# Kernel optimization log

Hardware: AMD Instinct MI355X
Metric: run time of the kernel (lower is better)

The kernel has to match this reference:

```python
import jax, jax.numpy as jnp
import numpy as np

N = 8192       # node_num
F_IN = 256     # src_feature
F_OUT = 128    # out_feature
NEG_SLOPE = 0.2  # standard GAT leakyrelu slope
MASK_VAL = -1e12


def setup_inputs() -> dict:
    key = jax.random.key(0)
    k1, k2, k3, k4, k5, k6 = jax.random.split(key, 6)
    x = jax.random.normal(k1, (N, F_IN), dtype=jnp.float32)
    adj = jax.random.randint(k2, (N, N), 0, 2, dtype=jnp.int32)  # 0/1 adjacency mask
    # xavier-uniform-like scales
    W = jax.random.normal(k3, (F_IN, F_OUT), dtype=jnp.float32) * np.float32(1.0 / np.sqrt(F_IN))
    a1 = jax.random.normal(k4, (F_OUT,), dtype=jnp.float32) * np.float32(0.1)  # att[:F_OUT]
    a2 = jax.random.normal(k5, (F_OUT,), dtype=jnp.float32) * np.float32(0.1)  # att[F_OUT:]
    bias = jax.random.normal(k6, (F_OUT,), dtype=jnp.float32) * np.float32(0.1)
    return {"x": x, "adj": adj, "W": W, "a1": a1, "a2": a2, "bias": bias}


def reference(x, adj, W, a1, a2, bias):
    # h = x @ W1  (src_h == dst_h for int src_dst_feature)
    h = x @ W  # [N, F_OUT]
    # e[i,j] = leakyrelu(att^T [h_i || h_j]) decomposed as (h@a1)_i + (h@a2)_j
    s_src = h @ a1  # [N]
    s_dst = h @ a2  # [N]
    e = jax.nn.leaky_relu(s_src[:, None] + s_dst[None, :], NEG_SLOPE)  # [N, N]
    masked = jnp.where(adj > 0, e, jnp.float32(MASK_VAL))
    attention = jax.nn.softmax(masked, axis=1)  # [N, N]
    # dropout in eval mode = identity; aggregate neighbor features
    out = attention @ h + bias  # [N, F_OUT]
    return out
```

## Files before the change

kernel.cpp:

```cpp
#include <hip/hip_runtime.h>
#include <cstdint>
#include <cstddef>

#define NN 8192
#define FIN 256
#define FOUT 128
#define SLOPE 0.2f
#define SHIFT 8.0f

typedef float f32x4 __attribute__((ext_vector_type(4)));
typedef __bf16 bf16x8 __attribute__((ext_vector_type(8)));
typedef int i32x4 __attribute__((ext_vector_type(4)));
typedef unsigned int u32x4 __attribute__((ext_vector_type(4)));
typedef unsigned int u32x2 __attribute__((ext_vector_type(2)));

__device__ __forceinline__ unsigned short f2bf(float f) {
  return __builtin_bit_cast(unsigned short, (__bf16)f);
}
__device__ __forceinline__ float bf2f(unsigned short u) {
  return (float)__builtin_bit_cast(__bf16, u);
}

__device__ __forceinline__ void async_cp16(void* lds, const void* g) {
  __builtin_amdgcn_global_load_lds(
      (const __attribute__((address_space(1))) void*)g,
      (__attribute__((address_space(3))) void*)lds, 16, 0, 0);
}

__global__ __launch_bounds__(256, 4) void k_hw(const float* __restrict__ x,
                                               const float* __restrict__ W,
                                               const float* __restrict__ a1,
                                               const float* __restrict__ a2,
                                               unsigned short* __restrict__ ht,
                                               float* __restrict__ Etab,
                                               unsigned short* __restrict__ FbfF,
                                               unsigned short* __restrict__ FbfF2) {
  __shared__ float xs[8][256];
  __shared__ unsigned short tile[128][8];
  const int tid = threadIdx.x;
  const int rowbase = blockIdx.x * 8;

  #pragma unroll
  for (int it = 0; it < 2; ++it) {
    int fi = it * 1024 + tid * 4;
    int r = fi >> 8, k = fi & 255;
    *(f32x4*)&xs[r][k] = *(const f32x4*)(x + (size_t)(rowbase + r) * FIN + k);
  }
  __syncthreads();

  const int r = tid >> 5;
  const int cg = tid & 31;
  f32x4 acc = {0.f, 0.f, 0.f, 0.f};

  #pragma unroll 8
  for (int k = 0; k < FIN; ++k) {
    f32x4 wv = *(const f32x4*)(W + k * FOUT + cg * 4);
    float xv = xs[r][k];
    acc[0] += xv * wv[0];
    acc[1] += xv * wv[1];
    acc[2] += xv * wv[2];
    acc[3] += xv * wv[3];
  }

  #pragma unroll
  for (int c = 0; c < 4; ++c) tile[cg * 4 + c][r] = f2bf(acc[c]);

  f32x4 av1 = *(const f32x4*)(a1 + cg * 4);
  f32x4 av2 = *(const f32x4*)(a2 + cg * 4);
  float s1 = acc[0] * av1[0] + acc[1] * av1[1] + acc[2] * av1[2] + acc[3] * av1[3];
  float s2 = acc[0] * av2[0] + acc[1] * av2[1] + acc[2] * av2[2] + acc[3] * av2[3];
  #pragma unroll
  for (int off = 16; off > 0; off >>= 1) {
    s1 += __shfl_xor(s1, off, 64);
    s2 += __shfl_xor(s2, off, 64);
  }
  if (cg == 0) {
    const int row = rowbase + r;
    float c0 = s1 + SHIFT;
    float c = fmaxf(c0, SLOPE * c0);
    Etab[(size_t)row * 2]     = __expf(s1 - c);
    Etab[(size_t)row * 2 + 1] = __expf(SLOPE * s1 - c);
    FbfF[row]  = f2bf(__expf(s2));
    FbfF2[row] = f2bf(__expf(SLOPE * s2));
  }
  __syncthreads();

  if (tid < 128) {
    u32x4 v = *(const u32x4*)&tile[tid][0];
    *(u32x4*)(ht + (size_t)tid * NN + rowbase) = v;
  }
}

__global__ __launch_bounds__(256, 2) void k_gat(const int* __restrict__ adj,
                                                const unsigned short* __restrict__ ht,
                                                const float* __restrict__ Etab,
                                                const unsigned short* __restrict__ FbfF,
                                                const unsigned short* __restrict__ FbfF2,
                                                const float* __restrict__ bias,
                                                float* __restrict__ out) {
  __shared__ int sA[2][16 * 64];
  __shared__ unsigned short sH[2][128 * 64];
  __shared__ unsigned short sF[2][128];
  __shared__ unsigned short sAF[2][1024];

  const int tid = threadIdx.x;
  const int wave = tid >> 6;
  const int lane = tid & 63;
  const int quad = lane >> 4;
  const int m = lane & 15;
  const int rowbase = blockIdx.x * 16;

  bf16x8 pm, pinv, pones;
  #pragma unroll
  for (int jj = 0; jj < 8; ++jj) {
    pm[jj] = (__bf16)(float)m;
    pinv[jj] = (__bf16)0.03125f;
    pones[jj] = (__bf16)1.0f;
  }
  f32x4 z = {0.f, 0.f, 0.f, 0.f};
  f32x4 rp = __builtin_amdgcn_mfma_f32_16x16x32_bf16(pm, pinv, z, 0, 0, 0);
  f32x4 cp = __builtin_amdgcn_mfma_f32_16x16x32_bf16(pinv, pm, z, 0, 0, 0);
  int rowmap[4], colmap[4];
  #pragma unroll
  for (int r = 0; r < 4; ++r) {
    rowmap[r] = ((int)(rp[r] + 0.5f)) & 15;
    colmap[r] = ((int)(cp[r] + 0.5f)) & 15;
  }

  const int b_half = tid & 1;
  const int b_lane = (tid >> 1) & 63;
  const int b_k32  = tid >> 7;
  const int b_m    = b_lane & 15;
  const int b_quad = b_lane >> 4;
  const int b_jl   = b_k32 * 32 + b_quad * 8 + b_half * 4;
  const int b_slot = (b_jl >> 2) ^ b_m;
  const float Eb  = Etab[(size_t)(rowbase + b_m) * 2];
  const float E2b = Etab[(size_t)(rowbase + b_m) * 2 + 1];

  const int t0 = wave * 2, t1 = wave * 2 + 1;
  f32x4 acc0 = z, acc1 = z, den = z;

  const unsigned short* srcH[4];
  #pragma unroll
  for (int il = 0; il < 4; ++il) {
    const int i = wave * 4 + il;
    const int f = i * 8 + (lane >> 3);
    const int g = (lane & 7) ^ (lane >> 3);
    srcH[il] = ht + (size_t)f * NN + g * 8;
  }
  const int* srcA[2] = {nullptr, nullptr};
  int slotA[2] = {0, 0};
  if (wave >= 2) {
    #pragma unroll
    for (int q = 0; q < 2; ++q) {
      const int il = (wave - 2) * 2 + q;
      const int r = il * 4 + (lane >> 4);
      const int g = (lane & 15) ^ r;
      slotA[q] = il;
      srcA[q] = adj + (size_t)(rowbase + r) * NN + g * 4;
    }
  }
  const unsigned short* srcF = nullptr;
  if (wave == 1) {
    srcF = (lane < 8) ? (FbfF + lane * 8) : (FbfF2 + (lane - 8) * 8);
  }

  auto stage = [&](int b) {
    #pragma unroll
    for (int il = 0; il < 4; ++il) {
      async_cp16(&sH[b][(wave * 4 + il) * 512], srcH[il]);
      srcH[il] += 64;
    }
    if (wave >= 2) {
      #pragma unroll
      for (int q = 0; q < 2; ++q) {
        async_cp16(&sA[b][slotA[q] * 256], srcA[q]);
        srcA[q] += 64;
      }
    } else if (wave == 1 && lane < 16) {
      async_cp16(&sF[b][0], srcF);
      srcF += 64;
    }
  };

  stage(0);

  for (int c = 0; c < 128; ++c) {
    const int cs = c & 1, ns = cs ^ 1;

    __syncthreads();
    if (c + 1 < 128) stage(ns);

    {
      i32x4 av = *(const i32x4*)&sA[cs][b_m * 64 + b_slot * 4];
      unsigned long long fq = *(const unsigned long long*)&sF[cs][b_jl];
      unsigned long long gq = *(const unsigned long long*)&sF[cs][64 + b_jl];
      unsigned afp0 = 0, afp1 = 0;
      #pragma unroll
      for (int e = 0; e < 4; ++e) {
        const float F = bf2f((unsigned short)(fq >> (16 * e)));
        const float G = bf2f((unsigned short)(gq >> (16 * e)));
        const float w = fmaxf(Eb * F, E2b * G);
        const unsigned wb = av[e] ? (unsigned)f2bf(w) : 0u;
        if (e < 2) afp0 |= wb << (16 * e);
        else       afp1 |= wb << (16 * (e - 2));
      }
      u32x2 pkt; pkt[0] = afp0; pkt[1] = afp1;
      *(u32x2*)&sAF[cs][tid * 4] = pkt;
    }

    __builtin_amdgcn_s_waitcnt(0xC07F);
    __builtin_amdgcn_s_barrier();

    #pragma unroll
    for (int k32 = 0; k32 < 2; ++k32) {
      bf16x8 af = __builtin_bit_cast(bf16x8,
          *(const u32x4*)&sAF[cs][k32 * 512 + lane * 8]);
      const int s0 = (k32 * 4 + quad) ^ (m & 7);
      bf16x8 b0 = __builtin_bit_cast(bf16x8,
          *(const u32x4*)&sH[cs][(t0 * 16 + m) * 64 + s0 * 8]);
      bf16x8 b1 = __builtin_bit_cast(bf16x8,
          *(const u32x4*)&sH[cs][(t1 * 16 + m) * 64 + s0 * 8]);
      acc0 = __builtin_amdgcn_mfma_f32_16x16x32_bf16(af, b0, acc0, 0, 0, 0);
      acc1 = __builtin_amdgcn_mfma_f32_16x16x32_bf16(af, b1, acc1, 0, 0, 0);
      den  = __builtin_amdgcn_mfma_f32_16x16x32_bf16(af, pones, den, 0, 0, 0);
    }
  }

  #pragma unroll
  for (int r = 0; r < 4; ++r) {
    const float inv = 1.0f / den[r];
    const int orow = rowbase + rowmap[r];
    const int c0 = t0 * 16 + colmap[r];
    const int c1 = t1 * 16 + colmap[r];
    out[(size_t)orow * FOUT + c0] = acc0[r] * inv + bias[c0];
    out[(size_t)orow * FOUT + c1] = acc1[r] * inv + bias[c1];
  }
}

extern "C" void kernel_launch(void* const* d_in, const int* in_sizes, int n_in,
                              void* d_out, int out_size, void* d_ws, size_t ws_size,
                              hipStream_t stream) {
  const float* x    = (const float*)d_in[0];
  const int*   adj  = (const int*)d_in[1];
  const float* W    = (const float*)d_in[2];
  const float* a1   = (const float*)d_in[3];
  const float* a2   = (const float*)d_in[4];
  const float* bias = (const float*)d_in[5];
  float* out = (float*)d_out;

  char* ws = (char*)d_ws;
  unsigned short* ht = (unsigned short*)ws;
  float* Etab = (float*)(ws + (size_t)2 * 1024 * 1024);
  unsigned short* FbfF =
      (unsigned short*)(ws + (size_t)2 * 1024 * 1024 + 64 * 1024);
  unsigned short* FbfF2 = FbfF + NN;

  k_hw<<<NN / 8, 256, 0, stream>>>(x, W, a1, a2, ht, Etab, FbfF, FbfF2);
  k_gat<<<NN / 16, 256, 0, stream>>>(adj, ht, Etab, FbfF, FbfF2, bias, out);
}
```

Before: 480.1 us.

## Process 32 rows per block with 512 threads and load h tiles directly into registers

The attention-aggregation kernel now handles 32 output rows per block with 8 waves. Each wave owns 16 output features and loads its bf16 h fragment straight from global memory into registers, prefetched one chunk ahead, instead of staging h through shared memory. This halves how often h is re-read per output row and removes the shared-memory h buffer and its LDS reads. In exchange there are fewer blocks (256 instead of 512, occupancy 1 block of 512 threads), and the direct global loads are uncoalesced row-strided reads whose latency is hidden only by the one-step register prefetch.

```diff
diff --git a/kernel.cpp b/kernel.cpp
--- a/kernel.cpp
+++ b/kernel.cpp
@@ -91,24 +91,23 @@
   }
 }
 
-__global__ __launch_bounds__(256, 2) void k_gat(const int* __restrict__ adj,
+__global__ __launch_bounds__(512, 1) void k_gat(const int* __restrict__ adj,
                                                 const unsigned short* __restrict__ ht,
                                                 const float* __restrict__ Etab,
                                                 const unsigned short* __restrict__ FbfF,
                                                 const unsigned short* __restrict__ FbfF2,
                                                 const float* __restrict__ bias,
                                                 float* __restrict__ out) {
-  __shared__ int sA[2][16 * 64];
-  __shared__ unsigned short sH[2][128 * 64];
+  __shared__ int sA[2][32 * 64];
   __shared__ unsigned short sF[2][128];
-  __shared__ unsigned short sAF[2][1024];
+  __shared__ unsigned short sAF[2][2048];
 
   const int tid = threadIdx.x;
   const int wave = tid >> 6;
   const int lane = tid & 63;
   const int quad = lane >> 4;
   const int m = lane & 15;
-  const int rowbase = blockIdx.x * 16;
+  const int rowbase = blockIdx.x * 32;
 
   bf16x8 pm, pinv, pones;
   #pragma unroll
@@ -129,70 +128,56 @@
 
   const int b_half = tid & 1;
   const int b_lane = (tid >> 1) & 63;
-  const int b_k32  = tid >> 7;
+  const int b_k32  = (tid >> 7) & 1;
+  const int b_rg   = tid >> 8;
   const int b_m    = b_lane & 15;
   const int b_quad = b_lane >> 4;
+  const int b_row  = b_rg * 16 + b_m;
   const int b_jl   = b_k32 * 32 + b_quad * 8 + b_half * 4;
   const int b_slot = (b_jl >> 2) ^ b_m;
-  const float Eb  = Etab[(size_t)(rowbase + b_m) * 2];
-  const float E2b = Etab[(size_t)(rowbase + b_m) * 2 + 1];
-
-  const int t0 = wave * 2, t1 = wave * 2 + 1;
-  f32x4 acc0 = z, acc1 = z, den = z;
-
-  const unsigned short* srcH[4];
-  #pragma unroll
-  for (int il = 0; il < 4; ++il) {
-    const int i = wave * 4 + il;
-    const int f = i * 8 + (lane >> 3);
-    const int g = (lane & 7) ^ (lane >> 3);
-    srcH[il] = ht + (size_t)f * NN + g * 8;
-  }
-  const int* srcA[2] = {nullptr, nullptr};
-  int slotA[2] = {0, 0};
-  if (wave >= 2) {
-    #pragma unroll
-    for (int q = 0; q < 2; ++q) {
-      const int il = (wave - 2) * 2 + q;
-      const int r = il * 4 + (lane >> 4);
-      const int g = (lane & 15) ^ r;
-      slotA[q] = il;
-      srcA[q] = adj + (size_t)(rowbase + r) * NN + g * 4;
-    }
-  }
+  const float Eb  = Etab[(size_t)(rowbase + b_row) * 2];
+  const float E2b = Etab[(size_t)(rowbase + b_row) * 2 + 1];
+
+  f32x4 acc[2] = {z, z}, den[2] = {z, z};
+
+  const int a_r = wave * 4 + (lane >> 4);
+  const int a_g = (lane & 15) ^ (a_r & 15);
+  const int* srcA = adj + (size_t)(rowbase + a_r) * NN + a_g * 4;
   const unsigned short* srcF = nullptr;
-  if (wave == 1) {
+  if (wave == 0) {
     srcF = (lane < 8) ? (FbfF + lane * 8) : (FbfF2 + (lane - 8) * 8);
   }
 
   auto stage = [&](int b) {
-    #pragma unroll
-    for (int il = 0; il < 4; ++il) {
-      async_cp16(&sH[b][(wave * 4 + il) * 512], srcH[il]);
-      srcH[il] += 64;
-    }
-    if (wave >= 2) {
-      #pragma unroll
-      for (int q = 0; q < 2; ++q) {
-        async_cp16(&sA[b][slotA[q] * 256], srcA[q]);
-        srcA[q] += 64;
-      }
-    } else if (wave == 1 && lane < 16) {
+    async_cp16(&sA[b][wave * 256], srcA);
+    srcA += 64;
+    if (wave == 0 && lane < 16) {
       async_cp16(&sF[b][0], srcF);
       srcF += 64;
     }
   };
 
+  const unsigned short* srcB = ht + (size_t)(wave * 16 + m) * NN + quad * 8;
+
   stage(0);
-
+  u32x4 bcur0 = *(const u32x4*)(srcB);
+  u32x4 bcur1 = *(const u32x4*)(srcB + 32);
+
+  #pragma unroll 2
   for (int c = 0; c < 128; ++c) {
     const int cs = c & 1, ns = cs ^ 1;
 
     __syncthreads();
     if (c + 1 < 128) stage(ns);
 
+    u32x4 bnxt0 = bcur0, bnxt1 = bcur1;
+    if (c + 1 < 128) {
+      bnxt0 = *(const u32x4*)(srcB + (c + 1) * 64);
+      bnxt1 = *(const u32x4*)(srcB + (c + 1) * 64 + 32);
+    }
+
     {
-      i32x4 av = *(const i32x4*)&sA[cs][b_m * 64 + b_slot * 4];
+      i32x4 av = *(const i32x4*)&sA[cs][b_row * 64 + b_slot * 4];
       unsigned long long fq = *(const unsigned long long*)&sF[cs][b_jl];
       unsigned long long gq = *(const unsigned long long*)&sF[cs][64 + b_jl];
       unsigned afp0 = 0, afp1 = 0;
@@ -214,27 +199,29 @@
 
     #pragma unroll
     for (int k32 = 0; k32 < 2; ++k32) {
-      bf16x8 af = __builtin_bit_cast(bf16x8,
-          *(const u32x4*)&sAF[cs][k32 * 512 + lane * 8]);
-      const int s0 = (k32 * 4 + quad) ^ (m & 7);
-      bf16x8 b0 = __builtin_bit_cast(bf16x8,
-          *(const u32x4*)&sH[cs][(t0 * 16 + m) * 64 + s0 * 8]);
-      bf16x8 b1 = __builtin_bit_cast(bf16x8,
-          *(const u32x4*)&sH[cs][(t1 * 16 + m) * 64 + s0 * 8]);
-      acc0 = __builtin_amdgcn_mfma_f32_16x16x32_bf16(af, b0, acc0, 0, 0, 0);
-      acc1 = __builtin_amdgcn_mfma_f32_16x16x32_bf16(af, b1, acc1, 0, 0, 0);
-      den  = __builtin_amdgcn_mfma_f32_16x16x32_bf16(af, pones, den, 0, 0, 0);
-    }
-  }
-
-  #pragma unroll
-  for (int r = 0; r < 4; ++r) {
-    const float inv = 1.0f / den[r];
-    const int orow = rowbase + rowmap[r];
-    const int c0 = t0 * 16 + colmap[r];
-    const int c1 = t1 * 16 + colmap[r];
-    out[(size_t)orow * FOUT + c0] = acc0[r] * inv + bias[c0];
-    out[(size_t)orow * FOUT + c1] = acc1[r] * inv + bias[c1];
+      const bf16x8 bf = __builtin_bit_cast(bf16x8, k32 ? bcur1 : bcur0);
+      #pragma unroll
+      for (int rg = 0; rg < 2; ++rg) {
+        bf16x8 af = __builtin_bit_cast(bf16x8,
+            *(const u32x4*)&sAF[cs][rg * 1024 + k32 * 512 + lane * 8]);
+        acc[rg] = __builtin_amdgcn_mfma_f32_16x16x32_bf16(af, bf, acc[rg], 0, 0, 0);
+        den[rg] = __builtin_amdgcn_mfma_f32_16x16x32_bf16(af, pones, den[rg], 0, 0, 0);
+      }
+    }
+
+    bcur0 = bnxt0;
+    bcur1 = bnxt1;
+  }
+
+  #pragma unroll
+  for (int rg = 0; rg < 2; ++rg) {
+    #pragma unroll
+    for (int r = 0; r < 4; ++r) {
+      const float inv = 1.0f / den[rg][r];
+      const int orow = rowbase + rg * 16 + rowmap[r];
+      const int col = wave * 16 + colmap[r];
+      out[(size_t)orow * FOUT + col] = acc[rg][r] * inv + bias[col];
+    }
   }
 }
 
@@ -257,5 +244,5 @@
   unsigned short* FbfF2 = FbfF + NN;
 
   k_hw<<<NN / 8, 256, 0, stream>>>(x, W, a1, a2, ht, Etab, FbfF, FbfF2);
-  k_gat<<<NN / 16, 256, 0, stream>>>(adj, ht, Etab, FbfF, FbfF2, bias, out);
-}
+  k_gat<<<NN / 32, 512, 0, stream>>>(adj, ht, Etab, FbfF, FbfF2, bias, out);
+}
```

Result: slower. 500.3 us (+4.2%).
